# Kernel tuning notes

Measured on AMD Instinct MI355X. Metric: run time of the kernel, lower is better.

The kernel has to match this reference:

```python
import jax, jax.numpy as jnp
import numpy as np

B, S, D = 8, 512, 1024
F = 4 * D        # FFN hidden
E = 8            # num experts
SCALE = 0.02


def setup_inputs() -> dict:
    key = jax.random.key(0)
    ks = jax.random.split(key, 16)
    n = lambda k, shape, s=SCALE: (jax.random.normal(k, shape, dtype=jnp.float32) * s)
    task_ids = jax.random.randint(ks[15], (B,), 0, E)
    return {
        "hidden_states": jax.random.normal(ks[0], (B, S, D), dtype=jnp.float32),
        "ohe_task": jax.nn.one_hot(task_ids, E, dtype=jnp.float32),
        # base model (2-layer FFN) params
        "W1": n(ks[1], (D, F)), "b1": n(ks[2], (F,)),
        "W2": n(ks[3], (F, D)), "b2": n(ks[4], (D,)),
        # expert task vectors (expert_sd - base_sd), stacked over experts
        "T_W1": n(ks[5], (E, D, F)), "T_b1": n(ks[6], (E, F)),
        "T_W2": n(ks[7], (E, F, D)), "T_b2": n(ks[8], (E, D)),
        # gate: 2 hidden ReLU layers then linear to E
        "Wg1": n(ks[9], (D, D)), "bg1": jnp.zeros((D,), jnp.float32),
        "Wg2": n(ks[10], (D, D)), "bg2": jnp.zeros((D,), jnp.float32),
        "Wgo": n(ks[11], (D, E)), "bgo": jnp.zeros((E,), jnp.float32),
    }


def reference(hidden_states, ohe_task, W1, b1, W2, b2,
              T_W1, T_b1, T_W2, T_b2,
              Wg1, bg1, Wg2, bg2, Wgo, bgo):
    x = hidden_states  # [B,S,D]
    # --- router: per-token logits -> softmax over experts -> mean over seq ---
    h = jax.nn.relu(jnp.einsum("bsd,de->bse", x, Wg1) + bg1)
    h = jax.nn.relu(jnp.einsum("bsd,de->bse", h, Wg2) + bg2)
    logits = jnp.einsum("bsd,de->bse", h, Wgo) + bgo        # [B,S,E]
    gate_weights = jax.nn.softmax(logits, axis=-1).mean(axis=1)  # [B,E]
    # --- per-sample weighted merge of expert task vectors into base params ---
    coeff = gate_weights + ohe_task                          # [B,E]
    W1b = W1 + jnp.einsum("be,edf->bdf", coeff, T_W1)        # [B,D,F]
    b1b = b1 + coeff @ T_b1                                  # [B,F]
    W2b = W2 + jnp.einsum("be,efd->bfd", coeff, T_W2)        # [B,F,D]
    b2b = b2 + coeff @ T_b2                                  # [B,D]
    # --- batched functional forward through merged FFN ---
    hmid = jax.nn.gelu(jnp.einsum("bsd,bdf->bsf", x, W1b) + b1b[:, None, :],
                       approximate=False)
    out = jnp.einsum("bsf,bfd->bsd", hmid, W2b) + b2b[:, None, :]
    return out, gate_weights
```

## Files before the change

kernel.cpp:

```cpp
#include <hip/hip_runtime.h>
#include <hip/hip_bf16.h>

typedef __attribute__((ext_vector_type(8))) short s16x8;
typedef __attribute__((ext_vector_type(4))) float f32x4;

#define GLOAD_LDS16(gsrc, ldst) \
  __builtin_amdgcn_global_load_lds((const __attribute__((address_space(1))) void*)(gsrc), \
      (__attribute__((address_space(3))) void*)(ldst), 16, 0, 0)

__global__ __launch_bounds__(256) void cvt_bf16(const float* __restrict__ in,
                                                __hip_bfloat16* __restrict__ out, long n) {
  long i = ((long)blockIdx.x * 256 + threadIdx.x) * 4;
  if (i + 3 >= n) return;
  float4 v = *(const float4*)(in + i);
  __hip_bfloat16 tmp[4] = {__float2bfloat16(v.x), __float2bfloat16(v.y),
                           __float2bfloat16(v.z), __float2bfloat16(v.w)};
  *(ushort4*)((unsigned short*)out + i) = *(const ushort4*)tmp;
}

template<int NB>
__global__ __launch_bounds__(256) void merge_transpose(
    const float* __restrict__ Wb, const float* __restrict__ T,
    const float* __restrict__ coeff, __hip_bfloat16* __restrict__ Out,
    int K, int N, int nE) {
  int ntn = N >> 6;
  int k0 = (blockIdx.x / ntn) << 6;
  int n0 = (blockIdx.x % ntn) << 6;
  int t = threadIdx.x;
  long KN = (long)K * N;

  float4 accb[NB][4];
#pragma unroll
  for (int i = 0; i < 4; ++i) {
    int e = i * 256 + t; int kk = e >> 4, nn = (e & 15) << 2;
    float4 bv = *(const float4*)&Wb[(long)(k0 + kk) * N + n0 + nn];
#pragma unroll
    for (int b2 = 0; b2 < NB; ++b2) accb[b2][i] = bv;
  }
  for (int ex = 0; ex < nE; ++ex) {
    float c[NB];
#pragma unroll
    for (int b2 = 0; b2 < NB; ++b2) c[b2] = coeff[b2 * 8 + ex];
#pragma unroll
    for (int i = 0; i < 4; ++i) {
      int e = i * 256 + t; int kk = e >> 4, nn = (e & 15) << 2;
      float4 tv = *(const float4*)&T[(long)ex * KN + (long)(k0 + kk) * N + n0 + nn];
#pragma unroll
      for (int b2 = 0; b2 < NB; ++b2) {
        accb[b2][i].x += c[b2] * tv.x; accb[b2][i].y += c[b2] * tv.y;
        accb[b2][i].z += c[b2] * tv.z; accb[b2][i].w += c[b2] * tv.w;
      }
    }
  }
  __shared__ __hip_bfloat16 lds[64 * 66];
  for (int b2 = 0; b2 < NB; ++b2) {
    __syncthreads();
#pragma unroll
    for (int i = 0; i < 4; ++i) {
      int e = i * 256 + t; int kk = e >> 4, nn = (e & 15) << 2;
      lds[kk * 66 + nn + 0] = __float2bfloat16(accb[b2][i].x);
      lds[kk * 66 + nn + 1] = __float2bfloat16(accb[b2][i].y);
      lds[kk * 66 + nn + 2] = __float2bfloat16(accb[b2][i].z);
      lds[kk * 66 + nn + 3] = __float2bfloat16(accb[b2][i].w);
    }
    __syncthreads();
#pragma unroll
    for (int i = 0; i < 4; ++i) {
      int o = i * 256 + t; int n2 = o >> 4, k2 = (o & 15) << 2;
      __hip_bfloat16 tmp[4];
#pragma unroll
      for (int j = 0; j < 4; ++j) tmp[j] = lds[(k2 + j) * 66 + n2];
      *(ushort4*)((unsigned short*)&Out[(long)b2 * KN + (long)(n0 + n2) * K + k0 + k2]) =
          *(const ushort4*)tmp;
    }
  }
}

__global__ __launch_bounds__(256) void merge_bias(const float* __restrict__ base,
                                                  const float* __restrict__ T,
                                                  const float* __restrict__ coeff,
                                                  float* __restrict__ out, int n) {
  int b = blockIdx.y;
  int i = blockIdx.x * 256 + threadIdx.x;
  if (i >= n) return;
  float v = base[i];
#pragma unroll
  for (int e = 0; e < 8; ++e) v += coeff[b * 8 + e] * T[(long)e * n + i];
  out[(long)b * n + i] = v;
}

template<int MODE, int ACT, bool OUTBF>
__global__ __launch_bounds__(256, 2) void gemm_bt(
    const __hip_bfloat16* __restrict__ A, const __hip_bfloat16* __restrict__ BT,
    const float* __restrict__ bias, void* __restrict__ Out,
    int N, int K, long sA, long sB, long sBias, long sOut,
    int kLen, long ksOut) {
  int bid = blockIdx.x;
  int b, m, n, kc = 0;
  if (MODE == 0)      { b = blockIdx.y; m = (bid & 7) * 4 + ((bid >> 3) & 3); n = bid >> 5; }
  else if (MODE == 1) { b = bid & 7; int tile = bid >> 3; m = tile & 3; n = tile >> 2; }
  else                { b = bid & 7; int tile = bid >> 3; m = tile & 3; n = (tile >> 2) & 7; kc = tile >> 5; }
  int m0 = m << 7, n0 = n << 7;
  int kOff = kc * kLen;

  const __hip_bfloat16* Ab = A + (long)b * sA;
  const __hip_bfloat16* Bb = BT + (long)b * sB;

  __shared__ __align__(16) __hip_bfloat16 As[128 * 64];
  __shared__ __align__(16) __hip_bfloat16 Bs[128 * 64];

  int t = threadIdx.x;
  int lane = t & 63;
  int wid = t >> 6;
  int wm = wid >> 1, wn = wid & 1;
  int lr = lane & 15, kg = lane >> 4;

  f32x4 acc[4][4] = {};

  for (int kt = kOff; kt < kOff + kLen; kt += 64) {
#pragma unroll
    for (int is = 0; is < 4; ++is) {
      int ci = is * 256 + t;
      int row = ci >> 3, cpos = ci & 7;
      int csrc = cpos ^ (row & 7);
      GLOAD_LDS16(Ab + (long)(m0 + row) * K + kt + csrc * 8, &As[ci * 8]);
      GLOAD_LDS16(Bb + (long)(n0 + row) * K + kt + csrc * 8, &Bs[ci * 8]);
    }
    __syncthreads();
#pragma unroll
    for (int ks = 0; ks < 2; ++ks) {
      s16x8 af[4], bfr[4];
#pragma unroll
      for (int mi = 0; mi < 4; ++mi) {
        int row = wm * 64 + mi * 16 + lr;
        int c = (ks * 4 + kg) ^ (row & 7);
        af[mi] = *(const s16x8*)&As[row * 64 + c * 8];
      }
#pragma unroll
      for (int ni = 0; ni < 4; ++ni) {
        int row = wn * 64 + ni * 16 + lr;
        int c = (ks * 4 + kg) ^ (row & 7);
        bfr[ni] = *(const s16x8*)&Bs[row * 64 + c * 8];
      }
#pragma unroll
      for (int mi = 0; mi < 4; ++mi)
#pragma unroll
        for (int ni = 0; ni < 4; ++ni)
          acc[mi][ni] = __builtin_amdgcn_mfma_f32_16x16x32_bf16(bfr[ni], af[mi], acc[mi][ni], 0, 0, 0);
    }
    __syncthreads();
  }

#pragma unroll
  for (int mi = 0; mi < 4; ++mi) {
    int row = m0 + wm * 64 + mi * 16 + lr;
#pragma unroll
    for (int ni = 0; ni < 4; ++ni) {
      int colb = n0 + wn * 64 + ni * 16 + kg * 4;
      float bv4[4] = {0.f, 0.f, 0.f, 0.f};
      if (bias != nullptr) {
        float4 bb = *(const float4*)&bias[(long)b * sBias + colb];
        bv4[0] = bb.x; bv4[1] = bb.y; bv4[2] = bb.z; bv4[3] = bb.w;
      }
      float v[4];
#pragma unroll
      for (int j = 0; j < 4; ++j) {
        v[j] = acc[mi][ni][j] + bv4[j];
        if (ACT == 1) v[j] = fmaxf(v[j], 0.f);
        else if (ACT == 2) v[j] = 0.5f * v[j] * (1.f + erff(v[j] * 0.70710678118f));
      }
      long off = kc * ksOut + (long)b * sOut + (long)row * N + colb;
      if (OUTBF) {
        __hip_bfloat16 tmp[4] = {__float2bfloat16(v[0]), __float2bfloat16(v[1]),
                                 __float2bfloat16(v[2]), __float2bfloat16(v[3])};
        *(ushort4*)((unsigned short*)Out + off) = *(const ushort4*)tmp;
      } else {
        *(float4*)((float*)Out + off) = make_float4(v[0], v[1], v[2], v[3]);
      }
    }
  }
}

__global__ __launch_bounds__(256) void reduce2_bias(
    const __hip_bfloat16* __restrict__ p, const float* __restrict__ b2b,
    float* __restrict__ out, long ksOut) {
  long i = ((long)blockIdx.x * 256 + threadIdx.x) * 8;
  const unsigned short* ps = (const unsigned short*)p;
  ushort4 a0 = *(const ushort4*)(ps + i);
  ushort4 a1 = *(const ushort4*)(ps + i + 4);
  ushort4 c0 = *(const ushort4*)(ps + ksOut + i);
  ushort4 c1 = *(const ushort4*)(ps + ksOut + i + 4);
  int d = (int)(i & 1023);
  int b = (int)(i >> 19);
  const float* bp = b2b + (long)b * 1024 + d;
  float o[8];
  unsigned short av[8] = {a0.x, a0.y, a0.z, a0.w, a1.x, a1.y, a1.z, a1.w};
  unsigned short cv[8] = {c0.x, c0.y, c0.z, c0.w, c1.x, c1.y, c1.z, c1.w};
#pragma unroll
  for (int j = 0; j < 8; ++j) {
    __hip_bfloat16 ab = *(__hip_bfloat16*)&av[j], cb = *(__hip_bfloat16*)&cv[j];
    o[j] = __bfloat162float(ab) + __bfloat162float(cb) + bp[j];
  }
  *(float4*)(out + i) = make_float4(o[0], o[1], o[2], o[3]);
  *(float4*)(out + i + 4) = make_float4(o[4], o[5], o[6], o[7]);
}

__global__ __launch_bounds__(256) void router_logits(
    const __hip_bfloat16* __restrict__ Hg2, const float* __restrict__ Wgo,
    const float* __restrict__ bgo, float* __restrict__ probs) {
  int r = blockIdx.x;
  int t = threadIdx.x;
  float acc[8] = {};
#pragma unroll
  for (int j = 0; j < 4; ++j) {
    int k = j * 256 + t;
    float h = __bfloat162float(Hg2[(long)r * 1024 + k]);
    const float4* wp = (const float4*)&Wgo[k * 8];
    float4 w0 = wp[0], w1 = wp[1];
    acc[0] += h * w0.x; acc[1] += h * w0.y; acc[2] += h * w0.z; acc[3] += h * w0.w;
    acc[4] += h * w1.x; acc[5] += h * w1.y; acc[6] += h * w1.z; acc[7] += h * w1.w;
  }
#pragma unroll
  for (int off = 32; off >= 1; off >>= 1)
#pragma unroll
    for (int e = 0; e < 8; ++e) acc[e] += __shfl_down(acc[e], off);
  __shared__ float lds[4][8];
  int wid = t >> 6, lane = t & 63;
  if (lane == 0)
#pragma unroll
    for (int e = 0; e < 8; ++e) lds[wid][e] = acc[e];
  __syncthreads();
  if (t == 0) {
    float lg[8];
#pragma unroll
    for (int e = 0; e < 8; ++e) lg[e] = lds[0][e] + lds[1][e] + lds[2][e] + lds[3][e] + bgo[e];
    float mx = lg[0];
#pragma unroll
    for (int e = 1; e < 8; ++e) mx = fmaxf(mx, lg[e]);
    float s = 0.f;
#pragma unroll
    for (int e = 0; e < 8; ++e) { lg[e] = __expf(lg[e] - mx); s += lg[e]; }
    float inv = 1.f / s;
#pragma unroll
    for (int e = 0; e < 8; ++e) probs[(long)r * 8 + e] = lg[e] * inv;
  }
}

__global__ __launch_bounds__(256) void router_mean(
    const float* __restrict__ probs, const float* __restrict__ ohe,
    float* __restrict__ gate_out, float* __restrict__ coeff) {
  int b = blockIdx.x;
  int t = threadIdx.x;
  int e = t & 7, sg = t >> 3;
  float s = 0.f;
#pragma unroll
  for (int j = 0; j < 16; ++j)
    s += probs[((long)b * 512 + sg + j * 32) * 8 + e];
  __shared__ float lds[256];
  lds[t] = s;
  __syncthreads();
  if (t < 8) {
    float tot = 0.f;
#pragma unroll
    for (int g = 0; g < 32; ++g) tot += lds[g * 8 + t];
    float gw = tot / 512.f;
    gate_out[b * 8 + t] = gw;
    coeff[b * 8 + t] = gw + ohe[b * 8 + t];
  }
}

extern "C" void kernel_launch(void* const* d_in, const int* in_sizes, int n_in,
                              void* d_out, int out_size, void* d_ws, size_t ws_size,
                              hipStream_t stream) {
  const float* x    = (const float*)d_in[0];
  const float* ohe  = (const float*)d_in[1];
  const float* W1   = (const float*)d_in[2];
  const float* b1   = (const float*)d_in[3];
  const float* W2   = (const float*)d_in[4];
  const float* b2   = (const float*)d_in[5];
  const float* T_W1 = (const float*)d_in[6];
  const float* T_b1 = (const float*)d_in[7];
  const float* T_W2 = (const float*)d_in[8];
  const float* T_b2 = (const float*)d_in[9];
  const float* Wg1  = (const float*)d_in[10];
  const float* bg1  = (const float*)d_in[11];
  const float* Wg2  = (const float*)d_in[12];
  const float* bg2  = (const float*)d_in[13];
  const float* Wgo  = (const float*)d_in[14];
  const float* bgo  = (const float*)d_in[15];
  float* out = (float*)d_out;
  float* gate_out = out + (long)8 * 512 * 1024;

  char* w = (char*)d_ws;
  __hip_bfloat16* xb   = (__hip_bfloat16*)(w);
  __hip_bfloat16* Wg1T = (__hip_bfloat16*)(w + 8388608);
  __hip_bfloat16* Wg2T = (__hip_bfloat16*)(w + 10485760);
  __hip_bfloat16* Hg1  = (__hip_bfloat16*)(w + 12582912);
  __hip_bfloat16* Hg2  = (__hip_bfloat16*)(w + 20971520);
  float*          probs= (float*)(w + 29360128);
  float*          coeff= (float*)(w + 29491200);
  float*          b1b  = (float*)(w + 29492224);
  float*          b2b  = (float*)(w + 29623296);
  __hip_bfloat16* hmid = (__hip_bfloat16*)(w + 29656064);
  __hip_bfloat16* Wb   = (__hip_bfloat16*)(w + 63210496);
  __hip_bfloat16* part = (__hip_bfloat16*)(w);

  const long SSD = (long)512 * 1024;
  const long SSF = (long)512 * 4096;

  cvt_bf16<<<4096, 256, 0, stream>>>(x, xb, (long)8 * 512 * 1024);
  merge_transpose<1><<<16 * 16, 256, 0, stream>>>(Wg1, nullptr, nullptr, Wg1T, 1024, 1024, 0);
  merge_transpose<1><<<16 * 16, 256, 0, stream>>>(Wg2, nullptr, nullptr, Wg2T, 1024, 1024, 0);
  gemm_bt<0, 1, true><<<dim3(256, 1), 256, 0, stream>>>(xb, Wg1T, bg1, Hg1,
      1024, 1024, 0, 0, 0, 0, 1024, 0);
  gemm_bt<0, 1, true><<<dim3(256, 1), 256, 0, stream>>>(Hg1, Wg2T, bg2, Hg2,
      1024, 1024, 0, 0, 0, 0, 1024, 0);
  router_logits<<<4096, 256, 0, stream>>>(Hg2, Wgo, bgo, probs);
  router_mean<<<8, 256, 0, stream>>>(probs, ohe, gate_out, coeff);
  merge_bias<<<dim3(16, 8), 256, 0, stream>>>(b1, T_b1, coeff, b1b, 4096);
  merge_bias<<<dim3(4, 8), 256, 0, stream>>>(b2, T_b2, coeff, b2b, 1024);
  merge_transpose<8><<<16 * 64, 256, 0, stream>>>(W1, T_W1, coeff, Wb, 1024, 4096, 8);
  gemm_bt<1, 2, true><<<dim3(1024, 1), 256, 0, stream>>>(xb, Wb, b1b, hmid,
      4096, 1024, SSD, (long)4096 * 1024, 4096, SSF, 1024, 0);
  merge_transpose<8><<<64 * 16, 256, 0, stream>>>(W2, T_W2, coeff, Wb, 4096, 1024, 8);
  gemm_bt<2, 0, true><<<dim3(512, 1), 256, 0, stream>>>(hmid, Wb, nullptr, part,
      1024, 4096, SSF, (long)4096 * 1024, 0, SSD, 2048, (long)8 * 512 * 1024);
  reduce2_bias<<<2048, 256, 0, stream>>>(part, b2b, out, (long)8 * 512 * 1024);
}
```

Baseline: 265.7 us.

## Add 256x256-tile double-buffered GEMM kernel for FFN layer 1 with GELU epilogue

Replaces the generic 128x128 gemm_bt used for the first merged-FFN matmul with a dedicated kernel. The new kernel uses 256x256 output tiles, 512 threads and double-buffered LDS staging through global_load_lds, with explicit vmcnt waits so the next K-slice loads overlap with the current MFMA work. The aim is more operand reuse per LDS load and less exposed memory latency. The cost is 128KB of LDS per block, so only one block fits per CU. The grid shrinks to 256 blocks, roughly one wave across the device, which leaves no other block on the CU to hide latency and risks tail imbalance.

```diff
diff --git a/kernel.cpp b/kernel.cpp
--- a/kernel.cpp
+++ b/kernel.cpp
@@ -98,7 +98,6 @@
   int bid = blockIdx.x;
   int b, m, n, kc = 0;
   if (MODE == 0)      { b = blockIdx.y; m = (bid & 7) * 4 + ((bid >> 3) & 3); n = bid >> 5; }
-  else if (MODE == 1) { b = bid & 7; int tile = bid >> 3; m = tile & 3; n = tile >> 2; }
   else                { b = bid & 7; int tile = bid >> 3; m = tile & 3; n = (tile >> 2) & 7; kc = tile >> 5; }
   int m0 = m << 7, n0 = n << 7;
   int kOff = kc * kLen;
@@ -177,6 +176,107 @@
       } else {
         *(float4*)((float*)Out + off) = make_float4(v[0], v[1], v[2], v[3]);
       }
+    }
+  }
+}
+
+__global__ __launch_bounds__(512, 2) void gemm256_l1(
+    const __hip_bfloat16* __restrict__ A, const __hip_bfloat16* __restrict__ BT,
+    const float* __restrict__ bias, __hip_bfloat16* __restrict__ Out) {
+  int bid = blockIdx.x;
+  int b = bid & 7;
+  int tile = bid >> 3;
+  int m0 = (tile & 1) << 8;
+  int n0 = (tile >> 1) << 8;
+  const int K = 1024, N = 4096;
+
+  const __hip_bfloat16* Ab = A + (long)b * 512 * 1024;
+  const __hip_bfloat16* Bb = BT + (long)b * 4096 * 1024;
+  const float* biasb = bias + (long)b * 4096;
+
+  __shared__ __align__(16) __hip_bfloat16 As[2][256 * 64];
+  __shared__ __align__(16) __hip_bfloat16 Bs[2][256 * 64];
+
+  int t = threadIdx.x;
+  int lane = t & 63;
+  int wid = t >> 6;
+  int wm = wid >> 2;
+  int wn = wid & 3;
+  int lr = lane & 15, kg = lane >> 4;
+
+  f32x4 acc[8][4] = {};
+
+  auto stage = [&](int buf, int kt) {
+#pragma unroll
+    for (int is = 0; is < 4; ++is) {
+      int ci = is * 512 + t;
+      int row = ci >> 3, cpos = ci & 7;
+      int csrc = cpos ^ (row & 7);
+      GLOAD_LDS16(Ab + (long)(m0 + row) * K + kt + csrc * 8, &As[buf][ci * 8]);
+    }
+#pragma unroll
+    for (int is = 0; is < 4; ++is) {
+      int ci = is * 512 + t;
+      int row = ci >> 3, cpos = ci & 7;
+      int csrc = cpos ^ (row & 7);
+      GLOAD_LDS16(Bb + (long)(n0 + row) * K + kt + csrc * 8, &Bs[buf][ci * 8]);
+    }
+  };
+
+  auto compute = [&](int buf) {
+#pragma unroll
+    for (int ks = 0; ks < 2; ++ks) {
+      s16x8 af[8], bfr[4];
+#pragma unroll
+      for (int mi = 0; mi < 8; ++mi) {
+        int row = wm * 128 + mi * 16 + lr;
+        int c = (ks * 4 + kg) ^ (row & 7);
+        af[mi] = *(const s16x8*)&As[buf][row * 64 + c * 8];
+      }
+#pragma unroll
+      for (int ni = 0; ni < 4; ++ni) {
+        int row = wn * 64 + ni * 16 + lr;
+        int c = (ks * 4 + kg) ^ (row & 7);
+        bfr[ni] = *(const s16x8*)&Bs[buf][row * 64 + c * 8];
+      }
+#pragma unroll
+      for (int mi = 0; mi < 8; ++mi)
+#pragma unroll
+        for (int ni = 0; ni < 4; ++ni)
+          acc[mi][ni] = __builtin_amdgcn_mfma_f32_16x16x32_bf16(bfr[ni], af[mi], acc[mi][ni], 0, 0, 0);
+    }
+  };
+
+  const int nk = 16;
+  stage(0, 0);
+  for (int it = 0; it < nk; ++it) {
+    if (it + 1 < nk) {
+      stage((it + 1) & 1, (it + 1) << 6);
+      asm volatile("s_waitcnt vmcnt(8)" ::: "memory");
+    } else {
+      asm volatile("s_waitcnt vmcnt(0)" ::: "memory");
+    }
+    asm volatile("s_barrier" ::: "memory");
+    compute(it & 1);
+    asm volatile("s_barrier" ::: "memory");
+  }
+
+#pragma unroll
+  for (int mi = 0; mi < 8; ++mi) {
+    int row = m0 + wm * 128 + mi * 16 + lr;
+#pragma unroll
+    for (int ni = 0; ni < 4; ++ni) {
+      int colb = n0 + wn * 64 + ni * 16 + kg * 4;
+      float4 bb = *(const float4*)&biasb[colb];
+      float v[4] = {acc[mi][ni][0] + bb.x, acc[mi][ni][1] + bb.y,
+                    acc[mi][ni][2] + bb.z, acc[mi][ni][3] + bb.w};
+#pragma unroll
+      for (int j = 0; j < 4; ++j)
+        v[j] = 0.5f * v[j] * (1.f + erff(v[j] * 0.70710678118f));
+      long off = (long)b * 512 * 4096 + (long)row * N + colb;
+      __hip_bfloat16 tmp[4] = {__float2bfloat16(v[0]), __float2bfloat16(v[1]),
+                               __float2bfloat16(v[2]), __float2bfloat16(v[3])};
+      *(ushort4*)((unsigned short*)Out + off) = *(const ushort4*)tmp;
     }
   }
 }
@@ -320,8 +420,7 @@
   merge_bias<<<dim3(16, 8), 256, 0, stream>>>(b1, T_b1, coeff, b1b, 4096);
   merge_bias<<<dim3(4, 8), 256, 0, stream>>>(b2, T_b2, coeff, b2b, 1024);
   merge_transpose<8><<<16 * 64, 256, 0, stream>>>(W1, T_W1, coeff, Wb, 1024, 4096, 8);
-  gemm_bt<1, 2, true><<<dim3(1024, 1), 256, 0, stream>>>(xb, Wb, b1b, hmid,
-      4096, 1024, SSD, (long)4096 * 1024, 4096, SSF, 1024, 0);
+  gemm256_l1<<<dim3(256, 1), 512, 0, stream>>>(xb, Wb, b1b, hmid);
   merge_transpose<8><<<64 * 16, 256, 0, stream>>>(W2, T_W2, coeff, Wb, 4096, 1024, 8);
   gemm_bt<2, 0, true><<<dim3(512, 1), 256, 0, stream>>>(hmid, Wb, nullptr, part,
       1024, 4096, SSF, (long)4096 * 1024, 0, SSD, 2048, (long)8 * 512 * 1024);
```

New measurement: 271.9 us. 1.02x slower.
